# Performance work log

Hardware: AMD Instinct MI355X
Metric: run time of the kernel (lower is better)

Reference implementation:

```python
import jax, jax.numpy as jnp
import numpy as np

HIDDEN = 4096
N_HEADS = 32
N_KV_HEADS = 8
HEAD_DIM = HIDDEN // N_HEADS  # 128
Q_SIZE = N_HEADS * HEAD_DIM
KV_SIZE = N_KV_HEADS * HEAD_DIM
ROPE_THETA = 10000.0
EPS = 1e-5
SCALE = HEAD_DIM ** -0.5


def _headwise_layernorm(x, weight, eps):
    # x: [B,S,H,D], weight: [H,D]; LayerNorm over last dim (head_dim), fp32 math
    xf = x.astype(jnp.float32)
    mean = xf.mean(-1, keepdims=True)
    var = jnp.square(xf - mean).mean(-1, keepdims=True)
    y = (xf - mean) * jax.lax.rsqrt(var + eps)
    return (weight.astype(jnp.float32) * y).astype(x.dtype)


def _rope_gptj(x, positions):
    # non-neox (GPT-J) style: rotate interleaved pairs. x: [B,S,H,D]
    half = HEAD_DIM // 2
    inv_freq = 1.0 / (ROPE_THETA ** (jnp.arange(0, HEAD_DIM, 2, dtype=jnp.float32) / HEAD_DIM))
    ang = positions.astype(jnp.float32)[..., None] * inv_freq  # [B,S,half]
    cos = jnp.cos(ang)[:, :, None, :]  # [B,S,1,half]
    sin = jnp.sin(ang)[:, :, None, :]
    x1 = x[..., 0::2]
    x2 = x[..., 1::2]
    o1 = x1 * cos - x2 * sin
    o2 = x2 * cos + x1 * sin
    # re-interleave
    out = jnp.stack([o1, o2], axis=-1).reshape(x.shape)
    return out.astype(x.dtype)


def setup_inputs() -> dict:
    key = jax.random.key(0)
    k1, k2, k3, k4 = jax.random.split(key, 4)
    B, S = 2, 2048
    positions = jnp.tile(jnp.arange(S, dtype=jnp.int32)[None, :], (B, 1))
    hidden_states = jax.random.normal(k1, (B, S, HIDDEN), dtype=jnp.float32)
    Wqkv = jax.random.normal(k2, (HIDDEN, Q_SIZE + 2 * KV_SIZE), dtype=jnp.float32) * (HIDDEN ** -0.5)
    Wo = jax.random.normal(k3, (Q_SIZE, HIDDEN), dtype=jnp.float32) * (Q_SIZE ** -0.5)
    kq, kk = jax.random.split(k4)
    q_norm_w = jnp.ones((N_HEADS, HEAD_DIM), jnp.float32) + 0.02 * jax.random.normal(kq, (N_HEADS, HEAD_DIM))
    k_norm_w = jnp.ones((N_KV_HEADS, HEAD_DIM), jnp.float32) + 0.02 * jax.random.normal(kk, (N_KV_HEADS, HEAD_DIM))
    return {"positions": positions, "hidden_states": hidden_states, "Wqkv": Wqkv,
            "q_norm_w": q_norm_w, "k_norm_w": k_norm_w, "Wo": Wo}


def reference(positions, hidden_states, Wqkv, q_norm_w, k_norm_w, Wo):
    B, S, _ = hidden_states.shape
    qkv = hidden_states @ Wqkv  # [B,S,Q+2KV]
    q, k, v = jnp.split(qkv, [Q_SIZE, Q_SIZE + KV_SIZE], axis=-1)
    q = q.reshape(B, S, N_HEADS, HEAD_DIM)
    k = k.reshape(B, S, N_KV_HEADS, HEAD_DIM)
    v = v.reshape(B, S, N_KV_HEADS, HEAD_DIM)
    # per-head qk-norm
    q = _headwise_layernorm(q, q_norm_w, EPS)
    k = _headwise_layernorm(k, k_norm_w, EPS)
    # non-neox RoPE
    q = _rope_gptj(q, positions)
    k = _rope_gptj(k, positions)
    # GQA: repeat kv heads
    n_rep = N_HEADS // N_KV_HEADS
    k = jnp.repeat(k, n_rep, axis=2)  # [B,S,H,D]
    v = jnp.repeat(v, n_rep, axis=2)
    scores = jnp.einsum('bqhd,bkhd->bhqk', q, k) * SCALE
    causal = jnp.tril(jnp.ones((S, S), dtype=bool))
    scores = jnp.where(causal[None, None], scores, jnp.finfo(scores.dtype).min)
    probs = jax.nn.softmax(scores, axis=-1)
    attn = jnp.einsum('bhqk,bkhd->bqhd', probs, v).reshape(B, S, Q_SIZE)
    return attn @ Wo
```

## Files before the change

### kernel.cpp

```cpp
#include <hip/hip_runtime.h>
#include <hip/hip_bf16.h>
#include <cstdint>

typedef unsigned short u16;
typedef unsigned int u32;
typedef __attribute__((ext_vector_type(8))) short bf16x8;
typedef __attribute__((ext_vector_type(4))) float f32x4;
typedef __attribute__((ext_vector_type(16))) float f32x16;
typedef __attribute__((ext_vector_type(4))) unsigned int u32x4;

#define HIDDEN 4096
#define NH 32
#define NKV 8
#define HD 128
#define QSZ 4096
#define KVSZ 1024
#define QKV_N 6144
#define SEQ 2048
#define NB 2
#define NTOK (NB*SEQ)
#define ATT_SCALE 0.08838834764831845f
#define LOG2E 1.4426950408889634f
#define LN_EPS 1e-5f
#define THRD 12.0f

__device__ __forceinline__ u16 f2bf(float f) {
  union { float f; u32 u; } a; a.f = f;
  u32 r = a.u + 0x7fffu + ((a.u >> 16) & 1u);
  return (u16)(r >> 16);
}
__device__ __forceinline__ float bf2f(u16 h) {
  union { u32 u; float f; } a; a.u = ((u32)h) << 16;
  return a.f;
}

__device__ __forceinline__ void gload_lds16(const void* g, void* l) {
  __builtin_amdgcn_global_load_lds(
      (const __attribute__((address_space(1))) void*)g,
      (__attribute__((address_space(3))) void*)l,
      16, 0, 0);
}

__global__ __launch_bounds__(256)
void conv_f32_bf16(const float* __restrict__ in, u16* __restrict__ out, int n8) {
  int i = blockIdx.x * 256 + threadIdx.x;
  if (i >= n8) return;
  const float4* p = (const float4*)in + (size_t)i * 2;
  float4 v0 = p[0], v1 = p[1];
  u32x4 o;
  o.x = (u32)f2bf(v0.x) | ((u32)f2bf(v0.y) << 16);
  o.y = (u32)f2bf(v0.z) | ((u32)f2bf(v0.w) << 16);
  o.z = (u32)f2bf(v1.x) | ((u32)f2bf(v1.y) << 16);
  o.w = (u32)f2bf(v1.z) | ((u32)f2bf(v1.w) << 16);
  ((u32x4*)out)[i] = o;
}

__global__ __launch_bounds__(256)
void transp_f32_bf16(const float* __restrict__ in, u16* __restrict__ out, int R, int C) {
  __shared__ float tile[32][33];
  int c0 = blockIdx.x << 5, r0 = blockIdx.y << 5;
  int tx = threadIdx.x & 31, ty = threadIdx.x >> 5;
  #pragma unroll
  for (int j = 0; j < 32; j += 8)
    tile[ty + j][tx] = in[(long)(r0 + ty + j) * C + c0 + tx];
  __syncthreads();
  #pragma unroll
  for (int j = 0; j < 32; j += 8)
    out[(long)(c0 + ty + j) * R + r0 + tx] = f2bf(tile[tx][ty + j]);
}

template<typename OutT>
__global__ __launch_bounds__(256)
void gemm_bt(const u16* __restrict__ A, const u16* __restrict__ Bt, OutT* __restrict__ C,
             int M, int N, int K) {
  __shared__ u16 As[128 * 32];
  __shared__ u16 Bs[128 * 32];
  const int t = threadIdx.x;
  const int lane = t & 63, wave = t >> 6;
  const int wm = wave >> 1, wn = wave & 1;
  const int bm = blockIdx.y, bn = blockIdx.x;
  f32x4 acc[4][4] = {};
  const int srow = t >> 2, schunk = t & 3;
  const u16* Ag = A + (long)(bm * 128 + srow) * K + schunk * 8;
  const u16* Bg = Bt + (long)(bn * 128 + srow) * K + schunk * 8;
  char* AsB = (char*)As + wave * 1024;
  char* BsB = (char*)Bs + wave * 1024;
  const int lrow = lane & 15;
  const int lkB = (lane >> 4) * 16;

  for (int k0 = 0; k0 < K; k0 += 32) {
    __syncthreads();
    gload_lds16(Ag + k0, AsB);
    gload_lds16(Ag + 64 * (long)K + k0, AsB + 4096);
    gload_lds16(Bg + k0, BsB);
    gload_lds16(Bg + 64 * (long)K + k0, BsB + 4096);
    __syncthreads();
    bf16x8 a[4], b[4];
    #pragma unroll
    for (int i = 0; i < 4; ++i) {
      a[i] = *(const bf16x8*)((const char*)As + (wm * 64 + i * 16 + lrow) * 64 + lkB);
      b[i] = *(const bf16x8*)((const char*)Bs + (wn * 64 + i * 16 + lrow) * 64 + lkB);
    }
    #pragma unroll
    for (int i = 0; i < 4; ++i)
      #pragma unroll
      for (int j = 0; j < 4; ++j)
        acc[i][j] = __builtin_amdgcn_mfma_f32_16x16x32_bf16(a[i], b[j], acc[i][j], 0, 0, 0);
  }
  const int r0 = bm * 128 + wm * 64 + (lane >> 4) * 4;
  const int c0 = bn * 128 + wn * 64 + lrow;
  #pragma unroll
  for (int i = 0; i < 4; ++i)
    #pragma unroll
    for (int j = 0; j < 4; ++j)
      #pragma unroll
      for (int r = 0; r < 4; ++r) {
        long row = r0 + i * 16 + r;
        long col = c0 + j * 16;
        float v = acc[i][j][r];
        if constexpr (sizeof(OutT) == 2) C[row * N + col] = f2bf(v);
        else                             C[row * N + col] = v;
      }
}

__device__ __forceinline__ void ln_rope_head(const u16* __restrict__ src,
                                             const float* __restrict__ wgt,
                                             u16* __restrict__ dst,
                                             int lane, float sa, float ca, float scale) {
  u32 xr = *(const u32*)(src + 2 * lane);
  float x1 = bf2f((u16)(xr & 0xffffu)), x2 = bf2f((u16)(xr >> 16));
  float ssum = x1 + x2;
  #pragma unroll
  for (int off = 1; off < 64; off <<= 1) ssum += __shfl_xor(ssum, off);
  float mean = ssum * (1.0f / 128.0f);
  float e1 = x1 - mean, e2 = x2 - mean;
  float vv = e1 * e1 + e2 * e2;
  #pragma unroll
  for (int off = 1; off < 64; off <<= 1) vv += __shfl_xor(vv, off);
  float rstd = rsqrtf(vv * (1.0f / 128.0f) + LN_EPS);
  float y1 = e1 * rstd * wgt[2 * lane];
  float y2 = e2 * rstd * wgt[2 * lane + 1];
  float o1 = (y1 * ca - y2 * sa) * scale;
  float o2 = (y2 * ca + y1 * sa) * scale;
  *(u32*)(dst + 2 * lane) = (u32)f2bf(o1) | ((u32)f2bf(o2) << 16);
}

__global__ __launch_bounds__(512)
void ln_rope(const u16* __restrict__ qkv, const int* __restrict__ pos,
             const float* __restrict__ qw, const float* __restrict__ kw,
             u16* __restrict__ qo, u16* __restrict__ ko) {
  const int s = blockIdx.x, b = blockIdx.y;
  const int t = threadIdx.x, lane = t & 63, w = t >> 6;
  const long base = (long)(b * SEQ + s) * QKV_N;
  const int p = pos[b * SEQ + s];
  const float expo = (float)(2 * lane) * (1.0f / 128.0f);
  const float inv_freq = exp2f(-expo * 13.287712379549449f);
  float sa, ca;
  sincosf((float)p * inv_freq, &sa, &ca);
  #pragma unroll
  for (int hh = 0; hh < 4; ++hh) {
    int h = w + hh * 8;
    ln_rope_head(qkv + base + h * HD, qw + h * HD,
                 qo + (((long)b * NH + h) * SEQ + s) * HD, lane, sa, ca,
                 ATT_SCALE * LOG2E);
  }
  ln_rope_head(qkv + base + QSZ + w * HD, kw + w * HD,
               ko + (((long)b * NKV + w) * SEQ + s) * HD, lane, sa, ca, 1.0f);
}

__global__ __launch_bounds__(256)
void v_transp(const u16* __restrict__ qkv, u16* __restrict__ vt) {
  __shared__ u16 tile[32][33];
  int s0 = blockIdx.x * 32, d0 = blockIdx.y * 32;
  int bk = blockIdx.z;
  int b = bk >> 3, kvh = bk & 7;
  int tx = threadIdx.x & 31, ty = threadIdx.x >> 5;
  const u16* src = qkv + ((long)(b * SEQ) + s0) * QKV_N + QSZ + KVSZ + kvh * HD + d0;
  #pragma unroll
  for (int j = 0; j < 32; j += 8)
    tile[ty + j][tx] = src[(long)(ty + j) * QKV_N + tx];
  __syncthreads();
  u16* dst = vt + (((long)bk) * HD + d0) * SEQ + s0;
  #pragma unroll
  for (int j = 0; j < 32; j += 8)
    dst[(long)(ty + j) * SEQ + tx] = tile[tx][ty + j];
}

__global__ __launch_bounds__(512, 2)
void flash_attn2(const u16* __restrict__ Qg, const u16* __restrict__ Kg,
                 const u16* __restrict__ Vtg, u16* __restrict__ Og) {
  const int lin = blockIdx.x;
  const int b = lin >> 8;
  const int rem = lin & 255;
  const int h = rem >> 3;
  const int q3 = rem & 7;
  const int qt = b ? (7 - q3) : q3;
  const int kvh = h >> 2;
  const int t = threadIdx.x, lane = t & 63, w = t >> 6;
  const int hh = lane >> 5, l31 = lane & 31;
  const int wq0 = qt * 256 + w * 32;
  const int q = wq0 + l31;

  __shared__ u16 Klds[2][64 * 128];
  __shared__ u16 Vlds[2][128 * 64];

  const u16* Qbase = Qg + (((long)b * NH + h) * SEQ + q) * HD + hh * 8;
  bf16x8 qf[8];
  #pragma unroll
  for (int ks = 0; ks < 8; ++ks) qf[ks] = *(const bf16x8*)(Qbase + ks * 16);

  f32x16 o[4];
  #pragma unroll
  for (int i = 0; i < 4; ++i)
    #pragma unroll
    for (int r = 0; r < 16; ++r) o[i][r] = 0.f;
  float m = -1e30f, l = 0.f;

  const u16* Kbase = Kg + ((long)b * NKV + kvh) * (long)SEQ * HD;
  const u16* Vtbase = Vtg + ((long)b * NKV + kvh) * (long)HD * SEQ;
  const int nt = qt * 4 + 4;

  auto STAGE = [&](int buf, int kt) {
    const int kv0 = kt * 64;
    #pragma unroll
    for (int i = 0; i < 2; ++i) {
      int c = t + i * 512;
      int kv = c >> 4, cc = c & 15;
      int cl = (cc & 8) | ((cc ^ kv) & 7);
      gload_lds16(Kbase + (long)(kv0 + kv) * HD + cl * 8,
                  (char*)(&Klds[buf][0]) + (i * 512 + w * 64) * 16);
    }
    #pragma unroll
    for (int i = 0; i < 2; ++i) {
      int c = t + i * 512;
      int d = c >> 3, cc = c & 7;
      int cl = cc ^ (d & 7);
      gload_lds16(Vtbase + (long)d * SEQ + kv0 + cl * 8,
                  (char*)(&Vlds[buf][0]) + (i * 512 + w * 64) * 16);
    }
  };

  STAGE(0, 0);
  __syncthreads();
  int cur = 0;
  for (int kt = 0; kt < nt; ++kt) {
    const int kv0 = kt * 64;
    if (kt + 1 < nt) STAGE(cur ^ 1, kt + 1);
    if (kv0 <= wq0 + 31) {
      const char* Kb = (const char*)(&Klds[cur][0]);
      const char* Vb = (const char*)(&Vlds[cur][0]);
      f32x16 st[2];
      #pragma unroll
      for (int tt = 0; tt < 2; ++tt)
        #pragma unroll
        for (int r = 0; r < 16; ++r) st[tt][r] = 0.f;
      __builtin_amdgcn_s_setprio(1);
      #pragma unroll
      for (int tt = 0; tt < 2; ++tt) {
        if (kv0 + tt * 32 <= wq0 + 31) {
          #pragma unroll
          for (int ks = 0; ks < 8; ++ks) {
            int ch = ks * 2 + hh;
            int pc = (ch & 8) | ((ch ^ l31) & 7);
            bf16x8 kf = *(const bf16x8*)(Kb + (tt * 32 + l31) * 256 + pc * 16);
            st[tt] = __builtin_amdgcn_mfma_f32_32x32x16_bf16(kf, qf[ks], st[tt], 0, 0, 0);
          }
        }
      }
      __builtin_amdgcn_s_setprio(0);
      if (kv0 + 63 > wq0) {
        #pragma unroll
        for (int tt = 0; tt < 2; ++tt)
          #pragma unroll
          for (int r = 0; r < 16; ++r) {
            int kva = kv0 + tt * 32 + (r & 3) + 8 * (r >> 2) + 4 * hh;
            if (kva > q) st[tt][r] = -1e30f;
          }
      }
      float p0 = -1e30f, p1 = -1e30f, p2 = -1e30f, p3 = -1e30f;
      #pragma unroll
      for (int tt = 0; tt < 2; ++tt)
        #pragma unroll
        for (int r = 0; r < 16; r += 4) {
          p0 = fmaxf(p0, st[tt][r]);
          p1 = fmaxf(p1, st[tt][r + 1]);
          p2 = fmaxf(p2, st[tt][r + 2]);
          p3 = fmaxf(p3, st[tt][r + 3]);
        }
      float mx = fmaxf(fmaxf(p0, p1), fmaxf(p2, p3));
      mx = fmaxf(mx, __shfl_xor(mx, 32));
      if (!__all(mx - m <= THRD)) {
        float mn = fmaxf(m, mx);
        float sc = exp2f(m - mn);
        m = mn;
        float scr[16];
        #pragma unroll
        for (int r = 0; r < 16; ++r)
          scr[r] = __shfl(sc, (r & 3) + 8 * (r >> 2) + 4 * hh);
        #pragma unroll
        for (int db = 0; db < 4; ++db)
          #pragma unroll
          for (int r = 0; r < 16; ++r) o[db][r] *= scr[r];
        l *= sc;
      }
      float s0 = 0.f, s1 = 0.f, s2 = 0.f, s3 = 0.f;
      #pragma unroll
      for (int tt = 0; tt < 2; ++tt)
        #pragma unroll
        for (int r = 0; r < 16; r += 4) {
          float e0 = exp2f(st[tt][r] - m);
          float e1 = exp2f(st[tt][r + 1] - m);
          float e2 = exp2f(st[tt][r + 2] - m);
          float e3 = exp2f(st[tt][r + 3] - m);
          st[tt][r] = e0; st[tt][r + 1] = e1; st[tt][r + 2] = e2; st[tt][r + 3] = e3;
          s0 += e0; s1 += e1; s2 += e2; s3 += e3;
        }
      float rs = (s0 + s1) + (s2 + s3);
      rs += __shfl_xor(rs, 32);
      l += rs;
      bf16x8 pa[4];
      #pragma unroll
      for (int k4 = 0; k4 < 4; ++k4) {
        int s8 = (k4 & 1) * 8, tt = k4 >> 1;
        u32 x0 = (u32)f2bf(st[tt][s8 + 0]) | ((u32)f2bf(st[tt][s8 + 1]) << 16);
        u32 x1 = (u32)f2bf(st[tt][s8 + 2]) | ((u32)f2bf(st[tt][s8 + 3]) << 16);
        u32 y0 = (u32)f2bf(st[tt][s8 + 4]) | ((u32)f2bf(st[tt][s8 + 5]) << 16);
        u32 y1 = (u32)f2bf(st[tt][s8 + 6]) | ((u32)f2bf(st[tt][s8 + 7]) << 16);
        u32 x0s = (u32)__shfl_xor((int)x0, 32), x1s = (u32)__shfl_xor((int)x1, 32);
        u32 y0s = (u32)__shfl_xor((int)y0, 32), y1s = (u32)__shfl_xor((int)y1, 32);
        union { u32 u[4]; bf16x8 v; } pk;
        pk.u[0] = hh ? y0s : x0;
        pk.u[1] = hh ? y1s : x1;
        pk.u[2] = hh ? y0 : x0s;
        pk.u[3] = hh ? y1 : x1s;
        pa[k4] = pk.v;
      }
      __builtin_amdgcn_s_setprio(1);
      #pragma unroll
      for (int k4 = 0; k4 < 4; ++k4)
        #pragma unroll
        for (int db = 0; db < 4; ++db) {
          int ch = k4 * 2 + hh;
          int pcc = ch ^ (l31 & 7);
          bf16x8 vf = *(const bf16x8*)(Vb + (db * 32 + l31) * 128 + pcc * 16);
          o[db] = __builtin_amdgcn_mfma_f32_32x32x16_bf16(pa[k4], vf, o[db], 0, 0, 0);
        }
      __builtin_amdgcn_s_setprio(0);
    }
    __syncthreads();
    cur ^= 1;
  }
  float linv = 1.0f / l;
  float li[16];
  #pragma unroll
  for (int r = 0; r < 16; ++r)
    li[r] = __shfl(linv, (r & 3) + 8 * (r >> 2) + 4 * hh);
  #pragma unroll
  for (int db = 0; db < 4; ++db)
    #pragma unroll
    for (int r = 0; r < 16; ++r) {
      int qr = wq0 + (r & 3) + 8 * (r >> 2) + 4 * hh;
      Og[((long)b * SEQ + qr) * QSZ + h * HD + db * 32 + l31] = f2bf(o[db][r] * li[r]);
    }
}

extern "C" void kernel_launch(void* const* d_in, const int* in_sizes, int n_in,
                              void* d_out, int out_size, void* d_ws, size_t ws_size,
                              hipStream_t stream) {
  const int*   positions = (const int*)d_in[0];
  const float* hidden    = (const float*)d_in[1];
  const float* Wqkv      = (const float*)d_in[2];
  const float* qnw       = (const float*)d_in[3];
  const float* knw       = (const float*)d_in[4];
  const float* Wo        = (const float*)d_in[5];
  float* out = (float*)d_out;
  char* ws = (char*)d_ws;
  const size_t MB = 1024 * 1024;
  u16* hbf   = (u16*)(ws + 0);
  u16* WqkvT = (u16*)(ws + 32 * MB);
  u16* qkvb  = (u16*)(ws + 80 * MB);
  u16* q_arr = (u16*)(ws + 0);
  u16* k_arr = (u16*)(ws + 32 * MB);
  u16* vt_arr= (u16*)(ws + 40 * MB);
  u16* WoT   = (u16*)(ws + 48 * MB);
  u16* Oarr  = (u16*)(ws + 80 * MB);

  conv_f32_bf16<<<dim3(NTOK * HIDDEN / 8 / 256), 256, 0, stream>>>(hidden, hbf, NTOK * HIDDEN / 8);
  transp_f32_bf16<<<dim3(QKV_N / 32, HIDDEN / 32), 256, 0, stream>>>(Wqkv, WqkvT, HIDDEN, QKV_N);
  gemm_bt<u16><<<dim3(QKV_N / 128, NTOK / 128), 256, 0, stream>>>(hbf, WqkvT, qkvb, NTOK, QKV_N, HIDDEN);
  ln_rope<<<dim3(SEQ, NB), 512, 0, stream>>>(qkvb, positions, qnw, knw, q_arr, k_arr);
  v_transp<<<dim3(SEQ / 32, HD / 32, NB * NKV), 256, 0, stream>>>(qkvb, vt_arr);
  transp_f32_bf16<<<dim3(HIDDEN / 32, QSZ / 32), 256, 0, stream>>>(Wo, WoT, QSZ, HIDDEN);
  flash_attn2<<<dim3(512), 512, 0, stream>>>(q_arr, k_arr, vt_arr, Oarr);
  gemm_bt<float><<<dim3(HIDDEN / 128, NTOK / 128), 256, 0, stream>>>(Oarr, WoT, out, NTOK, HIDDEN, QSZ);
}
```

Measured before the change: 674.1 us.

## Replace GEMM with triple-buffered 128x256 tile kernel using 32x32 MFMA

Both projection GEMMs now use a new kernel with 128x256 output tiles, 512 threads, a K-step of 64 and a three-stage LDS ring buffer. Global-to-LDS loads for the tile two steps ahead are issued while MFMAs run, and LDS columns are XOR-swizzled to avoid bank conflicts. It also switches to 32x32x16 MFMA, raises priority around MFMA blocks and remaps block IDs across XCD groups for L2 locality. This targets the single-buffered, barrier-bound loop of the old GEMM. The cost is 144KB of dynamic LDS per block, which may limit occupancy, plus more complex synchronisation.

```diff
diff --git a/kernel.cpp b/kernel.cpp
--- a/kernel.cpp
+++ b/kernel.cpp
@@ -70,54 +70,137 @@
 }
 
 template<typename OutT>
-__global__ __launch_bounds__(256)
-void gemm_bt(const u16* __restrict__ A, const u16* __restrict__ Bt, OutT* __restrict__ C,
-             int M, int N, int K) {
-  __shared__ u16 As[128 * 32];
-  __shared__ u16 Bs[128 * 32];
+__global__ __launch_bounds__(512, 2)
+void gemm_bt2(const u16* __restrict__ A, const u16* __restrict__ Bt,
+              OutT* __restrict__ C, int N, int K) {
+  extern __shared__ char smem[];
   const int t = threadIdx.x;
-  const int lane = t & 63, wave = t >> 6;
-  const int wm = wave >> 1, wn = wave & 1;
-  const int bm = blockIdx.y, bn = blockIdx.x;
-  f32x4 acc[4][4] = {};
-  const int srow = t >> 2, schunk = t & 3;
-  const u16* Ag = A + (long)(bm * 128 + srow) * K + schunk * 8;
-  const u16* Bg = Bt + (long)(bn * 128 + srow) * K + schunk * 8;
-  char* AsB = (char*)As + wave * 1024;
-  char* BsB = (char*)Bs + wave * 1024;
-  const int lrow = lane & 15;
-  const int lkB = (lane >> 4) * 16;
-
-  for (int k0 = 0; k0 < K; k0 += 32) {
-    __syncthreads();
-    gload_lds16(Ag + k0, AsB);
-    gload_lds16(Ag + 64 * (long)K + k0, AsB + 4096);
-    gload_lds16(Bg + k0, BsB);
-    gload_lds16(Bg + 64 * (long)K + k0, BsB + 4096);
-    __syncthreads();
-    bf16x8 a[4], b[4];
-    #pragma unroll
-    for (int i = 0; i < 4; ++i) {
-      a[i] = *(const bf16x8*)((const char*)As + (wm * 64 + i * 16 + lrow) * 64 + lkB);
-      b[i] = *(const bf16x8*)((const char*)Bs + (wn * 64 + i * 16 + lrow) * 64 + lkB);
-    }
-    #pragma unroll
-    for (int i = 0; i < 4; ++i)
-      #pragma unroll
-      for (int j = 0; j < 4; ++j)
-        acc[i][j] = __builtin_amdgcn_mfma_f32_16x16x32_bf16(a[i], b[j], acc[i][j], 0, 0, 0);
+  const int lane = t & 63, w = t >> 6;
+  const int wr = w >> 2, wc = w & 3;
+  const int l31 = lane & 31, l7 = lane & 7, g2 = lane >> 5;
+
+  const int nbn = N >> 8;
+  const int cpx = gridDim.x >> 3;
+  const int wg = (blockIdx.x & 7) * cpx + (blockIdx.x >> 3);
+  const int bm = wg / nbn, bn = wg - bm * nbn;
+
+  const int ciA0 = t, ciA1 = t + 512;
+  const u16* AgS0 = A + (long)(bm * 128 + (ciA0 >> 3)) * K + (((ciA0 & 7) ^ ((ciA0 >> 3) & 7)) << 3);
+  const u16* AgS1 = A + (long)(bm * 128 + (ciA1 >> 3)) * K + (((ciA1 & 7) ^ ((ciA1 >> 3) & 7)) << 3);
+  const u16* BgS0;
+  const u16* BgS1;
+  const u16* BgS2;
+  const u16* BgS3;
+  {
+    int ci0 = t, ci1 = t + 512, ci2 = t + 1024, ci3 = t + 1536;
+    BgS0 = Bt + (long)(bn * 256 + (ci0 >> 3)) * K + (((ci0 & 7) ^ ((ci0 >> 3) & 7)) << 3);
+    BgS1 = Bt + (long)(bn * 256 + (ci1 >> 3)) * K + (((ci1 & 7) ^ ((ci1 >> 3) & 7)) << 3);
+    BgS2 = Bt + (long)(bn * 256 + (ci2 >> 3)) * K + (((ci2 & 7) ^ ((ci2 >> 3) & 7)) << 3);
+    BgS3 = Bt + (long)(bn * 256 + (ci3 >> 3)) * K + (((ci3 & 7) ^ ((ci3 >> 3) & 7)) << 3);
   }
-  const int r0 = bm * 128 + wm * 64 + (lane >> 4) * 4;
-  const int c0 = bn * 128 + wn * 64 + lrow;
-  #pragma unroll
-  for (int i = 0; i < 4; ++i)
-    #pragma unroll
-    for (int j = 0; j < 4; ++j)
-      #pragma unroll
-      for (int r = 0; r < 4; ++r) {
-        long row = r0 + i * 16 + r;
-        long col = c0 + j * 16;
-        float v = acc[i][j][r];
+  const int dA0 = (w * 64) * 16;
+  const int dA1 = (512 + w * 64) * 16;
+  const int dB0 = 16384 + (w * 64) * 16;
+  const int dB1 = 16384 + (512 + w * 64) * 16;
+  const int dB2 = 16384 + (1024 + w * 64) * 16;
+  const int dB3 = 16384 + (1536 + w * 64) * 16;
+
+  const int arow0 = (wr * 64 + l31) * 128;
+  const int brow0 = 16384 + (wc * 64 + l31) * 128;
+
+  f32x16 acc[2][2];
+  #pragma unroll
+  for (int i = 0; i < 2; ++i)
+    #pragma unroll
+    for (int j = 0; j < 2; ++j)
+      #pragma unroll
+      for (int r = 0; r < 16; ++r) acc[i][j][r] = 0.f;
+
+  const int nt = K >> 6;
+  char* cbase = smem;
+  char* nbase = smem + 49152;
+  char* sbase = smem + 98304;
+
+  gload_lds16(AgS0, cbase + dA0);  gload_lds16(AgS1, cbase + dA1);
+  gload_lds16(BgS0, cbase + dB0);  gload_lds16(BgS1, cbase + dB1);
+  gload_lds16(BgS2, cbase + dB2);  gload_lds16(BgS3, cbase + dB3);
+  gload_lds16(AgS0 + 64, nbase + dA0);  gload_lds16(AgS1 + 64, nbase + dA1);
+  gload_lds16(BgS0 + 64, nbase + dB0);  gload_lds16(BgS1 + 64, nbase + dB1);
+  gload_lds16(BgS2 + 64, nbase + dB2);  gload_lds16(BgS3 + 64, nbase + dB3);
+  asm volatile("s_waitcnt vmcnt(6)" ::: "memory");
+  __builtin_amdgcn_s_barrier();
+  __builtin_amdgcn_sched_barrier(0);
+
+  for (int tt = 0; tt < nt; ++tt) {
+    const long sk = (long)((tt + 2 < nt) ? (tt + 2) : (nt - 1)) * 64;
+    bf16x8 aF[2][2], bF[2][2];
+    #pragma unroll
+    for (int kk = 0; kk < 2; ++kk) {
+      const int pcb = ((kk * 2 + g2) ^ l7) * 16;
+      #pragma unroll
+      for (int mf = 0; mf < 2; ++mf)
+        aF[kk][mf] = *(const bf16x8*)(cbase + arow0 + mf * 32 * 128 + pcb);
+      #pragma unroll
+      for (int nf = 0; nf < 2; ++nf)
+        bF[kk][nf] = *(const bf16x8*)(cbase + brow0 + nf * 32 * 128 + pcb);
+    }
+    gload_lds16(AgS0 + sk, sbase + dA0);
+    gload_lds16(AgS1 + sk, sbase + dA1);
+    __builtin_amdgcn_s_barrier();
+    __builtin_amdgcn_sched_barrier(0);
+    __builtin_amdgcn_s_setprio(1);
+    #pragma unroll
+    for (int kk = 0; kk < 2; ++kk)
+      #pragma unroll
+      for (int mf = 0; mf < 2; ++mf)
+        #pragma unroll
+        for (int nf = 0; nf < 2; ++nf)
+          acc[mf][nf] = __builtin_amdgcn_mfma_f32_32x32x16_bf16(aF[kk][mf], bF[kk][nf], acc[mf][nf], 0, 0, 0);
+    __builtin_amdgcn_s_setprio(0);
+    __builtin_amdgcn_sched_barrier(0);
+    __builtin_amdgcn_s_barrier();
+    __builtin_amdgcn_sched_barrier(0);
+    #pragma unroll
+    for (int kk = 0; kk < 2; ++kk) {
+      const int pcb = (((kk + 2) * 2 + g2) ^ l7) * 16;
+      #pragma unroll
+      for (int mf = 0; mf < 2; ++mf)
+        aF[kk][mf] = *(const bf16x8*)(cbase + arow0 + mf * 32 * 128 + pcb);
+      #pragma unroll
+      for (int nf = 0; nf < 2; ++nf)
+        bF[kk][nf] = *(const bf16x8*)(cbase + brow0 + nf * 32 * 128 + pcb);
+    }
+    gload_lds16(BgS0 + sk, sbase + dB0);
+    gload_lds16(BgS1 + sk, sbase + dB1);
+    gload_lds16(BgS2 + sk, sbase + dB2);
+    gload_lds16(BgS3 + sk, sbase + dB3);
+    asm volatile("s_waitcnt vmcnt(6)" ::: "memory");
+    __builtin_amdgcn_s_barrier();
+    __builtin_amdgcn_sched_barrier(0);
+    __builtin_amdgcn_s_setprio(1);
+    #pragma unroll
+    for (int kk = 0; kk < 2; ++kk)
+      #pragma unroll
+      for (int mf = 0; mf < 2; ++mf)
+        #pragma unroll
+        for (int nf = 0; nf < 2; ++nf)
+          acc[mf][nf] = __builtin_amdgcn_mfma_f32_32x32x16_bf16(aF[kk][mf], bF[kk][nf], acc[mf][nf], 0, 0, 0);
+    __builtin_amdgcn_s_setprio(0);
+    __builtin_amdgcn_sched_barrier(0);
+    __builtin_amdgcn_s_barrier();
+    __builtin_amdgcn_sched_barrier(0);
+    char* tmp = cbase; cbase = nbase; nbase = sbase; sbase = tmp;
+  }
+
+  #pragma unroll
+  for (int mf = 0; mf < 2; ++mf)
+    #pragma unroll
+    for (int nf = 0; nf < 2; ++nf)
+      #pragma unroll
+      for (int r = 0; r < 16; ++r) {
+        long row = bm * 128 + wr * 64 + mf * 32 + (r & 3) + 8 * (r >> 2) + 4 * g2;
+        long col = bn * 256 + wc * 64 + nf * 32 + l31;
+        float v = acc[mf][nf][r];
         if constexpr (sizeof(OutT) == 2) C[row * N + col] = f2bf(v);
         else                             C[row * N + col] = v;
       }
@@ -385,12 +468,18 @@
   u16* WoT   = (u16*)(ws + 48 * MB);
   u16* Oarr  = (u16*)(ws + 80 * MB);
 
+  const int GEMM_LDS = 3 * 49152;
+  (void)hipFuncSetAttribute((const void*)&gemm_bt2<u16>,
+        hipFuncAttributeMaxDynamicSharedMemorySize, GEMM_LDS);
+  (void)hipFuncSetAttribute((const void*)&gemm_bt2<float>,
+        hipFuncAttributeMaxDynamicSharedMemorySize, GEMM_LDS);
+
   conv_f32_bf16<<<dim3(NTOK * HIDDEN / 8 / 256), 256, 0, stream>>>(hidden, hbf, NTOK * HIDDEN / 8);
   transp_f32_bf16<<<dim3(QKV_N / 32, HIDDEN / 32), 256, 0, stream>>>(Wqkv, WqkvT, HIDDEN, QKV_N);
-  gemm_bt<u16><<<dim3(QKV_N / 128, NTOK / 128), 256, 0, stream>>>(hbf, WqkvT, qkvb, NTOK, QKV_N, HIDDEN);
+  gemm_bt2<u16><<<dim3((NTOK / 128) * (QKV_N / 256)), 512, GEMM_LDS, stream>>>(hbf, WqkvT, qkvb, QKV_N, HIDDEN);
   ln_rope<<<dim3(SEQ, NB), 512, 0, stream>>>(qkvb, positions, qnw, knw, q_arr, k_arr);
   v_transp<<<dim3(SEQ / 32, HD / 32, NB * NKV), 256, 0, stream>>>(qkvb, vt_arr);
   transp_f32_bf16<<<dim3(HIDDEN / 32, QSZ / 32), 256, 0, stream>>>(Wo, WoT, QSZ, HIDDEN);
   flash_attn2<<<dim3(512), 512, 0, stream>>>(q_arr, k_arr, vt_arr, Oarr);
-  gemm_bt<float><<<dim3(HIDDEN / 128, NTOK / 128), 256, 0, stream>>>(Oarr, WoT, out, NTOK, HIDDEN, QSZ);
-}
+  gemm_bt2<float><<<dim3((NTOK / 128) * (HIDDEN / 256)), 512, GEMM_LDS, stream>>>(Oarr, WoT, out, HIDDEN, QSZ);
+}
```

Result: faster. 618.7 us (-8.2%).

## Replace bf16 GEMM with 256x256 double-buffered, swizzled 32x32 MFMA kernel

Applied to the files above, without the earlier changes.

Replaces the single-buffered 128x128 GEMM with a 256x256-tile kernel using 512 threads and 32x32x16 bf16 MFMAs. Each K=64 step is split into two halves, and the next tile is prefetched into a second 64 KB LDS buffer while the current one is consumed. An XOR swizzle is meant to avoid LDS bank conflicts. The aim is higher MFMA utilisation and less global and LDS traffic per FLOP for both the QKV and output projections. The cost is 128 KB of LDS per block, which limits occupancy to one block per CU, and fewer blocks in the grid (256 to 384).

```diff
diff --git a/kernel.cpp b/kernel.cpp
--- a/kernel.cpp
+++ b/kernel.cpp
@@ -70,54 +70,107 @@
 }
 
 template<typename OutT>
-__global__ __launch_bounds__(256)
-void gemm_bt(const u16* __restrict__ A, const u16* __restrict__ Bt, OutT* __restrict__ C,
-             int M, int N, int K) {
-  __shared__ u16 As[128 * 32];
-  __shared__ u16 Bs[128 * 32];
+__global__ __launch_bounds__(512, 2)
+void gemm_bt3(const u16* __restrict__ A, const u16* __restrict__ Bt,
+              OutT* __restrict__ C, int N, int K) {
+  extern __shared__ char smem[];
   const int t = threadIdx.x;
-  const int lane = t & 63, wave = t >> 6;
-  const int wm = wave >> 1, wn = wave & 1;
+  const int lane = t & 63, w = t >> 6;
+  const int wr = w >> 2, wc = w & 3;
+  const int l31 = lane & 31, g2 = lane >> 5;
   const int bm = blockIdx.y, bn = blockIdx.x;
-  f32x4 acc[4][4] = {};
-  const int srow = t >> 2, schunk = t & 3;
-  const u16* Ag = A + (long)(bm * 128 + srow) * K + schunk * 8;
-  const u16* Bg = Bt + (long)(bn * 128 + srow) * K + schunk * 8;
-  char* AsB = (char*)As + wave * 1024;
-  char* BsB = (char*)Bs + wave * 1024;
-  const int lrow = lane & 15;
-  const int lkB = (lane >> 4) * 16;
-
-  for (int k0 = 0; k0 < K; k0 += 32) {
-    __syncthreads();
-    gload_lds16(Ag + k0, AsB);
-    gload_lds16(Ag + 64 * (long)K + k0, AsB + 4096);
-    gload_lds16(Bg + k0, BsB);
-    gload_lds16(Bg + 64 * (long)K + k0, BsB + 4096);
-    __syncthreads();
-    bf16x8 a[4], b[4];
-    #pragma unroll
-    for (int i = 0; i < 4; ++i) {
-      a[i] = *(const bf16x8*)((const char*)As + (wm * 64 + i * 16 + lrow) * 64 + lkB);
-      b[i] = *(const bf16x8*)((const char*)Bs + (wn * 64 + i * 16 + lrow) * 64 + lkB);
-    }
-    #pragma unroll
-    for (int i = 0; i < 4; ++i)
-      #pragma unroll
-      for (int j = 0; j < 4; ++j)
-        acc[i][j] = __builtin_amdgcn_mfma_f32_16x16x32_bf16(a[i], b[j], acc[i][j], 0, 0, 0);
+
+  const int sA0 = t, sA1 = t + 512;
+  const u16* pA0 = A  + (long)(bm * 256 + (sA0 >> 2)) * K + (((sA0 & 3) ^ ((sA0 >> 2) & 3)) << 3);
+  const u16* pA1 = A  + (long)(bm * 256 + (sA1 >> 2)) * K + (((sA1 & 3) ^ ((sA1 >> 2) & 3)) << 3);
+  const u16* pB0 = Bt + (long)(bn * 256 + (sA0 >> 2)) * K + (((sA0 & 3) ^ ((sA0 >> 2) & 3)) << 3);
+  const u16* pB1 = Bt + (long)(bn * 256 + (sA1 >> 2)) * K + (((sA1 & 3) ^ ((sA1 >> 2) & 3)) << 3);
+  const int dst0 = w * 1024;
+  const int dst1 = 8192 + w * 1024;
+
+  const int arow = wr * 128 + l31;
+  const int brow = wc * 64 + l31;
+
+  f32x16 acc[4][2];
+  #pragma unroll
+  for (int i = 0; i < 4; ++i)
+    #pragma unroll
+    for (int j = 0; j < 2; ++j)
+      #pragma unroll
+      for (int r = 0; r < 16; ++r) acc[i][j][r] = 0.f;
+
+  const int nt = K >> 6;
+  char* cb = smem;
+  char* sb = smem + 65536;
+
+  gload_lds16(pA0, cb + dst0);              gload_lds16(pA1, cb + dst1);
+  gload_lds16(pB0, cb + 32768 + dst0);      gload_lds16(pB1, cb + 32768 + dst1);
+  gload_lds16(pA0 + 32, cb + 16384 + dst0); gload_lds16(pA1 + 32, cb + 16384 + dst1);
+  gload_lds16(pB0 + 32, cb + 49152 + dst0); gload_lds16(pB1 + 32, cb + 49152 + dst1);
+  asm volatile("s_waitcnt vmcnt(4)" ::: "memory");
+  __builtin_amdgcn_s_barrier();
+  __builtin_amdgcn_sched_barrier(0);
+
+  #define READ_KK(dst, kkv) { \
+    const int u_ = (((kkv) * 2 + g2) >> 2) * 16384; \
+    const int p_ = (((((kkv) * 2 + g2) & 3) ^ (l31 & 3)) << 4); \
+    dst[0] = *(const bf16x8*)(cb + u_ + (arow      ) * 64 + p_); \
+    dst[1] = *(const bf16x8*)(cb + u_ + (arow + 32 ) * 64 + p_); \
+    dst[2] = *(const bf16x8*)(cb + u_ + (arow + 64 ) * 64 + p_); \
+    dst[3] = *(const bf16x8*)(cb + u_ + (arow + 96 ) * 64 + p_); \
+    dst[4] = *(const bf16x8*)(cb + 32768 + u_ + (brow     ) * 64 + p_); \
+    dst[5] = *(const bf16x8*)(cb + 32768 + u_ + (brow + 32) * 64 + p_); }
+  #define MFMA_KK(f) { \
+    __builtin_amdgcn_s_setprio(1); \
+    acc[0][0] = __builtin_amdgcn_mfma_f32_32x32x16_bf16(f[0], f[4], acc[0][0], 0, 0, 0); \
+    acc[0][1] = __builtin_amdgcn_mfma_f32_32x32x16_bf16(f[0], f[5], acc[0][1], 0, 0, 0); \
+    acc[1][0] = __builtin_amdgcn_mfma_f32_32x32x16_bf16(f[1], f[4], acc[1][0], 0, 0, 0); \
+    acc[1][1] = __builtin_amdgcn_mfma_f32_32x32x16_bf16(f[1], f[5], acc[1][1], 0, 0, 0); \
+    acc[2][0] = __builtin_amdgcn_mfma_f32_32x32x16_bf16(f[2], f[4], acc[2][0], 0, 0, 0); \
+    acc[2][1] = __builtin_amdgcn_mfma_f32_32x32x16_bf16(f[2], f[5], acc[2][1], 0, 0, 0); \
+    acc[3][0] = __builtin_amdgcn_mfma_f32_32x32x16_bf16(f[3], f[4], acc[3][0], 0, 0, 0); \
+    acc[3][1] = __builtin_amdgcn_mfma_f32_32x32x16_bf16(f[3], f[5], acc[3][1], 0, 0, 0); \
+    __builtin_amdgcn_s_setprio(0); }
+
+  for (int tt = 0; tt < nt; ++tt) {
+    const long sk = (long)((tt + 1 < nt) ? (tt + 1) : (nt - 1)) * 64;
+    bf16x8 f0[6], f1[6];
+    READ_KK(f0, 0);
+    gload_lds16(pA0 + sk, sb + dst0);
+    gload_lds16(pA1 + sk, sb + dst1);
+    MFMA_KK(f0);
+    READ_KK(f1, 1);
+    gload_lds16(pB0 + sk, sb + 32768 + dst0);
+    gload_lds16(pB1 + sk, sb + 32768 + dst1);
+    MFMA_KK(f1);
+    asm volatile("s_waitcnt vmcnt(4)" ::: "memory");
+    __builtin_amdgcn_s_barrier();
+    __builtin_amdgcn_sched_barrier(0);
+    READ_KK(f0, 2);
+    gload_lds16(pA0 + sk + 32, sb + 16384 + dst0);
+    gload_lds16(pA1 + sk + 32, sb + 16384 + dst1);
+    MFMA_KK(f0);
+    READ_KK(f1, 3);
+    gload_lds16(pB0 + sk + 32, sb + 49152 + dst0);
+    gload_lds16(pB1 + sk + 32, sb + 49152 + dst1);
+    MFMA_KK(f1);
+    asm volatile("s_waitcnt vmcnt(4)" ::: "memory");
+    __builtin_amdgcn_s_barrier();
+    __builtin_amdgcn_sched_barrier(0);
+    char* tmp = cb; cb = sb; sb = tmp;
   }
-  const int r0 = bm * 128 + wm * 64 + (lane >> 4) * 4;
-  const int c0 = bn * 128 + wn * 64 + lrow;
-  #pragma unroll
-  for (int i = 0; i < 4; ++i)
-    #pragma unroll
-    for (int j = 0; j < 4; ++j)
-      #pragma unroll
-      for (int r = 0; r < 4; ++r) {
-        long row = r0 + i * 16 + r;
-        long col = c0 + j * 16;
-        float v = acc[i][j][r];
+  #undef READ_KK
+  #undef MFMA_KK
+
+  #pragma unroll
+  for (int mf = 0; mf < 4; ++mf)
+    #pragma unroll
+    for (int nf = 0; nf < 2; ++nf)
+      #pragma unroll
+      for (int r = 0; r < 16; ++r) {
+        long row = bm * 256 + wr * 128 + mf * 32 + (r & 3) + 8 * (r >> 2) + 4 * g2;
+        long col = bn * 256 + wc * 64 + nf * 32 + l31;
+        float v = acc[mf][nf][r];
         if constexpr (sizeof(OutT) == 2) C[row * N + col] = f2bf(v);
         else                             C[row * N + col] = v;
       }
@@ -385,12 +438,18 @@
   u16* WoT   = (u16*)(ws + 48 * MB);
   u16* Oarr  = (u16*)(ws + 80 * MB);
 
+  const int GEMM_LDS = 2 * 65536;
+  (void)hipFuncSetAttribute((const void*)&gemm_bt3<u16>,
+        hipFuncAttributeMaxDynamicSharedMemorySize, GEMM_LDS);
+  (void)hipFuncSetAttribute((const void*)&gemm_bt3<float>,
+        hipFuncAttributeMaxDynamicSharedMemorySize, GEMM_LDS);
+
   conv_f32_bf16<<<dim3(NTOK * HIDDEN / 8 / 256), 256, 0, stream>>>(hidden, hbf, NTOK * HIDDEN / 8);
   transp_f32_bf16<<<dim3(QKV_N / 32, HIDDEN / 32), 256, 0, stream>>>(Wqkv, WqkvT, HIDDEN, QKV_N);
-  gemm_bt<u16><<<dim3(QKV_N / 128, NTOK / 128), 256, 0, stream>>>(hbf, WqkvT, qkvb, NTOK, QKV_N, HIDDEN);
+  gemm_bt3<u16><<<dim3(QKV_N / 256, NTOK / 256), 512, GEMM_LDS, stream>>>(hbf, WqkvT, qkvb, QKV_N, HIDDEN);
   ln_rope<<<dim3(SEQ, NB), 512, 0, stream>>>(qkvb, positions, qnw, knw, q_arr, k_arr);
   v_transp<<<dim3(SEQ / 32, HD / 32, NB * NKV), 256, 0, stream>>>(qkvb, vt_arr);
   transp_f32_bf16<<<dim3(HIDDEN / 32, QSZ / 32), 256, 0, stream>>>(Wo, WoT, QSZ, HIDDEN);
   flash_attn2<<<dim3(512), 512, 0, stream>>>(q_arr, k_arr, vt_arr, Oarr);
-  gemm_bt<float><<<dim3(HIDDEN / 128, NTOK / 128), 256, 0, stream>>>(Oarr, WoT, out, NTOK, HIDDEN, QSZ);
-}
+  gemm_bt3<float><<<dim3(HIDDEN / 256, NTOK / 256), 512, GEMM_LDS, stream>>>(Oarr, WoT, out, HIDDEN, QSZ);
+}
```

Result: faster. 608.9 us (-9.7%).
